# Optimization experiments

Measured on AMD Instinct MI355X. Metric: run time of the kernel, lower is better.

## Reference

```python
import jax, jax.numpy as jnp
import numpy as np

N_NODES = 50000
N_EDGES = 800000


def _sage_conv(h, ei, W_l, W_r, b_l):
    """PyG SAGEConv: lin_l(mean_{j->i} h_j) + lin_r(h_i). lin_l has bias, lin_r does not."""
    src, dst = ei[0], ei[1]
    # mean-aggregate raw features first (linear commutes with mean) to avoid [E, out] intermediates
    msum = jax.ops.segment_sum(h[src], dst, num_segments=N_NODES)          # [N, d]
    cnt = jax.ops.segment_sum(jnp.ones((ei.shape[1], 1), h.dtype), dst,
                              num_segments=N_NODES)                         # [N, 1]
    mean = msum / jnp.maximum(cnt, 1.0)
    return mean @ W_l + b_l + h @ W_r


def setup_inputs() -> dict:
    key = jax.random.key(0)
    ks = jax.random.split(key, 8)
    d_in, d_hid, d_out = 64, 64, 32
    return {
        "x": jax.random.normal(ks[0], (N_NODES, d_in), dtype=jnp.float32),
        "ei0": jax.random.randint(ks[1], (2, N_EDGES), 0, N_NODES, dtype=jnp.int32),
        "ei1": jax.random.randint(ks[2], (2, N_EDGES), 0, N_NODES, dtype=jnp.int32),
        "Wl": jax.random.normal(ks[3], (2, 2, d_in, d_hid), dtype=jnp.float32) * 0.05,
        "Wr": jax.random.normal(ks[4], (2, 2, d_in, d_hid), dtype=jnp.float32) * 0.05,
        "bl": jax.random.normal(ks[5], (2, 2, d_hid), dtype=jnp.float32) * 0.05,
        "lin_W": jax.random.normal(ks[6], (d_hid, d_out), dtype=jnp.float32) * 0.05,
        "lin_b": jax.random.normal(ks[7], (d_out,), dtype=jnp.float32) * 0.05,
    }


def reference(x, ei0, ei1, Wl, Wr, bl, lin_W, lin_b):
    edge_indices = (ei0, ei1)  # one edge_index per relation
    h = x
    for l in range(2):  # layers (structurally fixed)
        out = None
        for r, ei in enumerate(edge_indices):  # HeteroConv aggr='sum' over relations
            y = _sage_conv(h, ei, Wl[l, r], Wr[l, r], bl[l, r])
            out = y if out is None else out + y
        h = jax.nn.relu(out)
    return h @ lin_W + lin_b
```

## Files before the change

### kernel.cpp

```cpp
#include <hip/hip_runtime.h>

#define NN 50000
#define CAP 32
#define OVF_LDS 1024
#define SHARD_W 64
#define NSH 782
#define NPB 512

__device__ __forceinline__ unsigned short f2bf(float f) {
    unsigned u = __float_as_uint(f);
    u += 0x7fffu + ((u >> 16) & 1u);
    return (unsigned short)(u >> 16);
}
__device__ __forceinline__ float bf2f(unsigned short u) {
    return __uint_as_float(((unsigned)u) << 16);
}


__global__ __launch_bounds__(256) void shard_hist(
    const float* __restrict__ x, unsigned short* __restrict__ xb,
    const int* __restrict__ ei0, int E0,
    const int* __restrict__ ei1, int E1,
    unsigned short* __restrict__ hist16)
{
    int gtid = blockIdx.x * 256 + threadIdx.x;
    int gsz  = gridDim.x * 256;
    for (int i = gtid; i < NN * 16; i += gsz) {
        float4 v = ((const float4*)x)[i];
        ushort4 o;
        o.x = f2bf(v.x); o.y = f2bf(v.y); o.z = f2bf(v.z); o.w = f2bf(v.w);
        ((ushort4*)xb)[i] = o;
    }

    __shared__ unsigned lh[NSH];
    int local = blockIdx.x; int rel = 0;
    if (local >= NPB) { local -= NPB; rel = 1; }
    int pb = (local & 7) * (NPB / 8) + (local >> 3);
    const int* ei = rel ? ei1 : ei0;
    int E         = rel ? E1  : E0;
    int ce = (E + NPB - 1) / NPB;
    int lo = pb * ce, hi = min(lo + ce, E);

    for (int i = threadIdx.x; i < NSH; i += 256) lh[i] = 0;
    __syncthreads();
    for (int t = lo + threadIdx.x; t < hi; t += 256)
        atomicAdd(&lh[ei[E + t] >> 6], 1u);
    __syncthreads();
    for (int i = threadIdx.x; i < NSH; i += 256)
        hist16[((size_t)rel * NSH + i) * NPB + pb] = (unsigned short)lh[i];
}

__global__ __launch_bounds__(256) void total_pass(
    const unsigned short* __restrict__ hist16, int* __restrict__ tot)
{
    int gw = (blockIdx.x * 256 + threadIdx.x) >> 6;
    int lane = threadIdx.x & 63;
    if (gw >= 2 * NSH) return;
    uint4 v = ((const uint4*)(hist16 + (size_t)gw * NPB))[lane];
    unsigned s = (v.x & 0xffffu) + (v.x >> 16) + (v.y & 0xffffu) + (v.y >> 16)
               + (v.z & 0xffffu) + (v.z >> 16) + (v.w & 0xffffu) + (v.w >> 16);
    for (int off = 32; off; off >>= 1) s += __shfl_down(s, off);
    if (lane == 0) tot[gw] = (int)s;
}

__global__ __launch_bounds__(256) void scan_pass(
    const int* __restrict__ tot, int* __restrict__ sbase)
{
    __shared__ int ps[256];
    int t = threadIdx.x;
    int v[7];
    int s = 0;
    #pragma unroll
    for (int j = 0; j < 7; j++) {
        int i = t * 7 + j;
        v[j] = (i < 2 * NSH) ? tot[i] : 0;
        s += v[j];
    }
    ps[t] = s;
    __syncthreads();
    for (int off = 1; off < 256; off <<= 1) {
        int add = (t >= off) ? ps[t - off] : 0;
        __syncthreads();
        ps[t] += add;
        __syncthreads();
    }
    int run = (t == 0) ? 0 : ps[t - 1];
    #pragma unroll
    for (int j = 0; j < 7; j++) {
        int i = t * 7 + j;
        if (i < 2 * NSH) sbase[i] = run;
        run += v[j];
    }
    if (t == 255) sbase[2 * NSH] = run;
}

__global__ __launch_bounds__(256) void blockbase_pass(
    const unsigned short* __restrict__ hist16, const int* __restrict__ sbase,
    unsigned* __restrict__ pbase)
{
    int gw = (blockIdx.x * 256 + threadIdx.x) >> 6;
    int lane = threadIdx.x & 63;
    if (gw >= 2 * NSH) return;
    uint4 v = ((const uint4*)(hist16 + (size_t)gw * NPB))[lane];
    unsigned c[8] = {v.x & 0xffffu, v.x >> 16, v.y & 0xffffu, v.y >> 16,
                     v.z & 0xffffu, v.z >> 16, v.w & 0xffffu, v.w >> 16};
    unsigned lsum = 0;
    #pragma unroll
    for (int j = 0; j < 8; j++) lsum += c[j];
    unsigned incl = lsum;
    for (int off = 1; off < 64; off <<= 1) {
        unsigned n = __shfl_up(incl, off);
        if (lane >= off) incl += n;
    }
    unsigned run = (unsigned)sbase[gw] + incl - lsum;
    unsigned* prow = pbase + (size_t)gw * NPB + lane * 8;
    #pragma unroll
    for (int j = 0; j < 8; j++) { prow[j] = run; run += c[j]; }
}

__global__ __launch_bounds__(256) void partition_pass(
    const int* __restrict__ ei0, int E0,
    const int* __restrict__ ei1, int E1,
    const unsigned* __restrict__ pbase,
    unsigned* __restrict__ compact)
{
    __shared__ unsigned lbase[NSH];
    __shared__ unsigned lrank[NSH];
    int local = blockIdx.x; int rel = 0;
    if (local >= NPB) { local -= NPB; rel = 1; }
    int pb = (local & 7) * (NPB / 8) + (local >> 3);
    const int* ei = rel ? ei1 : ei0;
    int E         = rel ? E1  : E0;
    int ce = (E + NPB - 1) / NPB;
    int lo = pb * ce, hi = min(lo + ce, E);

    for (int i = threadIdx.x; i < NSH; i += 256) {
        lbase[i] = pbase[((size_t)rel * NSH + i) * NPB + pb];
        lrank[i] = 0;
    }
    __syncthreads();
    for (int t = lo + threadIdx.x; t < hi; t += 256) {
        int dst = ei[E + t];
        int src = ei[t];
        int s = dst >> 6;
        unsigned r = atomicAdd(&lrank[s], 1u);
        compact[lbase[s] + r] = ((unsigned)dst << 16) | (unsigned)src;
    }
}

__global__ __launch_bounds__(256) void aggregate_shard(
    const unsigned* __restrict__ compact, const int* __restrict__ sbase,
    const unsigned short* __restrict__ hb, unsigned short* __restrict__ agg)
{
    __shared__ unsigned short lbins[SHARD_W * CAP];
    __shared__ unsigned lcnt[SHARD_W];
    __shared__ unsigned lovf[OVF_LDS];
    __shared__ unsigned lovf_cnt;

    int bid = blockIdx.x;
    int rel = bid / NSH;
    int s   = bid - rel * NSH;
    int tid = threadIdx.x;
    int lane = tid & 63;
    int qtr = lane >> 4;
    int r   = lane & 15;
    int wid = tid >> 6;

    if (tid < SHARD_W) lcnt[tid] = 0;
    if (tid == 0) lovf_cnt = 0;
    __syncthreads();

    int base = sbase[bid];
    int tt   = sbase[bid + 1] - base;
    for (int j = tid; j < tt; j += 256) {
        unsigned e = compact[base + j];
        int loc = (int)(e >> 16) & (SHARD_W - 1);
        unsigned rr = atomicAdd(&lcnt[loc], 1u);
        if (rr < CAP) {
            lbins[loc * CAP + rr] = (unsigned short)(e & 0xffffu);
        } else {
            unsigned o = atomicAdd(&lovf_cnt, 1u);
            if (o < OVF_LDS) lovf[o] = ((unsigned)loc << 16) | (e & 0xffffu);
        }
    }
    __syncthreads();

    const uint2* hb64 = (const uint2*)hb;
    uint2* agg64 = (uint2*)agg;
    for (int t = 0; t < 16; ++t) {
        int loc = wid * 16 + t;
        int d = (int)lcnt[loc];
        int m = min(d, CAP);
        int idx = 0;
        if (lane < m) idx = lbins[loc * CAP + lane];
        float a0=0.f, a1=0.f, a2=0.f, a3=0.f;
        float b0=0.f, b1=0.f, b2=0.f, b3=0.f;
        int steps = (m + 3) >> 2;
        int j = 0;
        for (; j + 2 <= steps; j += 2) {
            int e0 = 4 * j + qtr;
            int e1 = 4 * (j + 1) + qtr;
            int s0 = __shfl(idx, e0 & 31);
            int s1 = __shfl(idx, e1 & 31);
            uint2 u0 = (e0 < m) ? hb64[(size_t)s0 * 16 + r] : make_uint2(0u, 0u);
            uint2 u1 = (e1 < m) ? hb64[(size_t)s1 * 16 + r] : make_uint2(0u, 0u);
            a0 += __uint_as_float(u0.x << 16); a1 += __uint_as_float(u0.x & 0xffff0000u);
            a2 += __uint_as_float(u0.y << 16); a3 += __uint_as_float(u0.y & 0xffff0000u);
            b0 += __uint_as_float(u1.x << 16); b1 += __uint_as_float(u1.x & 0xffff0000u);
            b2 += __uint_as_float(u1.y << 16); b3 += __uint_as_float(u1.y & 0xffff0000u);
        }
        for (; j < steps; ++j) {
            int e0 = 4 * j + qtr;
            int s0 = __shfl(idx, e0 & 31);
            uint2 u0 = (e0 < m) ? hb64[(size_t)s0 * 16 + r] : make_uint2(0u, 0u);
            a0 += __uint_as_float(u0.x << 16); a1 += __uint_as_float(u0.x & 0xffff0000u);
            a2 += __uint_as_float(u0.y << 16); a3 += __uint_as_float(u0.y & 0xffff0000u);
        }
        if (d > CAP) {
            int cnt = min((int)lovf_cnt, OVF_LDS);
            for (int e0 = 0; e0 < cnt; ++e0) {
                unsigned v = lovf[e0];
                if ((int)(v >> 16) == loc && qtr == 0) {
                    uint2 u = hb64[(size_t)(v & 0xffffu) * 16 + r];
                    a0 += __uint_as_float(u.x << 16); a1 += __uint_as_float(u.x & 0xffff0000u);
                    a2 += __uint_as_float(u.y << 16); a3 += __uint_as_float(u.y & 0xffff0000u);
                }
            }
        }
        a0 += b0; a1 += b1; a2 += b2; a3 += b3;
        a0 += __shfl_xor(a0, 16); a0 += __shfl_xor(a0, 32);
        a1 += __shfl_xor(a1, 16); a1 += __shfl_xor(a1, 32);
        a2 += __shfl_xor(a2, 16); a2 += __shfl_xor(a2, 32);
        a3 += __shfl_xor(a3, 16); a3 += __shfl_xor(a3, 32);
        int node = s * SHARD_W + loc;
        if (lane < 16 && node < NN) {
            float inv = 1.0f / (float)max(d, 1);
            uint2 o;
            o.x = (unsigned)f2bf(a0 * inv) | ((unsigned)f2bf(a1 * inv) << 16);
            o.y = (unsigned)f2bf(a2 * inv) | ((unsigned)f2bf(a3 * inv) << 16);
            agg64[((size_t)rel * NN + node) * 16 + r] = o;
        }
    }
}

#define RST 132
__global__ __launch_bounds__(256) void layer_gemm(
    const unsigned short* __restrict__ agg0, const unsigned short* __restrict__ agg1,
    const unsigned short* __restrict__ selfb,
    const float* __restrict__ Wl0, const float* __restrict__ Wl1,
    const float* __restrict__ Wr0, const float* __restrict__ Wr1,
    const float* __restrict__ b0, const float* __restrict__ b1,
    unsigned short* __restrict__ hb16)
{
    __shared__ float Wch[64 * 64];
    __shared__ float rowsT[64 * RST];
    __shared__ float bias[64];

    int tid = threadIdx.x;
    int base = blockIdx.x * 128;
    if (tid < 64) bias[tid] = b0[tid] + b1[tid];

    int j8 = (tid & 7) * 8;
    int n4 = (tid >> 3) * 4;

    float acc[4][8];
    #pragma unroll
    for (int i = 0; i < 4; i++)
        #pragma unroll
        for (int c = 0; c < 8; c++) acc[i][c] = 0.f;

    for (int chunk = 0; chunk < 3; chunk++) {
        const float* W = (chunk == 0) ? Wl0 : (chunk == 1) ? Wl1 : Wr0;
        const unsigned short* src = (chunk == 0) ? agg0 : (chunk == 1) ? agg1 : selfb;
        __syncthreads();
        #pragma unroll
        for (int r = 0; r < 4; r++) {
            int i = tid + 256 * r;
            float4 w = *(const float4*)&W[i * 4];
            if (chunk == 2) {
                float4 w2 = *(const float4*)&Wr1[i * 4];
                w.x += w2.x; w.y += w2.y; w.z += w2.z; w.w += w2.w;
            }
            *(float4*)&Wch[i * 4] = w;
        }
        #pragma unroll
        for (int r = 0; r < 8; r++) {
            int i = tid + 256 * r;
            int node = i >> 4;
            int k4 = (i & 15) * 4;
            int g = base + node;
            ushort4 u = make_ushort4(0, 0, 0, 0);
            if (g < NN) u = *(const ushort4*)&src[(size_t)g * 64 + k4];
            rowsT[(k4 + 0) * RST + node] = bf2f(u.x);
            rowsT[(k4 + 1) * RST + node] = bf2f(u.y);
            rowsT[(k4 + 2) * RST + node] = bf2f(u.z);
            rowsT[(k4 + 3) * RST + node] = bf2f(u.w);
        }
        __syncthreads();
        #pragma unroll 4
        for (int k = 0; k < 64; k++) {
            float4 wa = *(const float4*)&Wch[k * 64 + j8];
            float4 wb = *(const float4*)&Wch[k * 64 + j8 + 4];
            float4 rv = *(const float4*)&rowsT[k * RST + n4];
            float w[8] = {wa.x, wa.y, wa.z, wa.w, wb.x, wb.y, wb.z, wb.w};
            float rr[4] = {rv.x, rv.y, rv.z, rv.w};
            #pragma unroll
            for (int i = 0; i < 4; i++)
                #pragma unroll
                for (int c = 0; c < 8; c++)
                    acc[i][c] = fmaf(rr[i], w[c], acc[i][c]);
        }
    }

    #pragma unroll
    for (int i = 0; i < 4; i++) {
        int g = base + n4 + i;
        if (g < NN) {
            ushort4 p0, p1;
            p0.x = f2bf(fmaxf(acc[i][0] + bias[j8 + 0], 0.f));
            p0.y = f2bf(fmaxf(acc[i][1] + bias[j8 + 1], 0.f));
            p0.z = f2bf(fmaxf(acc[i][2] + bias[j8 + 2], 0.f));
            p0.w = f2bf(fmaxf(acc[i][3] + bias[j8 + 3], 0.f));
            p1.x = f2bf(fmaxf(acc[i][4] + bias[j8 + 4], 0.f));
            p1.y = f2bf(fmaxf(acc[i][5] + bias[j8 + 5], 0.f));
            p1.z = f2bf(fmaxf(acc[i][6] + bias[j8 + 6], 0.f));
            p1.w = f2bf(fmaxf(acc[i][7] + bias[j8 + 7], 0.f));
            *(ushort4*)&hb16[(size_t)g * 64 + j8]     = p0;
            *(ushort4*)&hb16[(size_t)g * 64 + j8 + 4] = p1;
        }
    }
}

__global__ __launch_bounds__(256) void layer_gemm_final(
    const unsigned short* __restrict__ agg0, const unsigned short* __restrict__ agg1,
    const unsigned short* __restrict__ selfb,
    const float* __restrict__ Wl0, const float* __restrict__ Wl1,
    const float* __restrict__ Wr0, const float* __restrict__ Wr1,
    const float* __restrict__ b0, const float* __restrict__ b1,
    const float* __restrict__ linW, const float* __restrict__ linb,
    float* __restrict__ out)
{
    __shared__ float Wch[64 * 64];
    __shared__ float rowsT[64 * RST];
    __shared__ float bias[64];

    int tid = threadIdx.x;
    int base = blockIdx.x * 128;
    if (tid < 64) bias[tid] = b0[tid] + b1[tid];

    int j8 = (tid & 7) * 8;
    int n4 = (tid >> 3) * 4;

    float acc[4][8];
    #pragma unroll
    for (int i = 0; i < 4; i++)
        #pragma unroll
        for (int c = 0; c < 8; c++) acc[i][c] = 0.f;

    for (int chunk = 0; chunk < 3; chunk++) {
        const float* W = (chunk == 0) ? Wl0 : (chunk == 1) ? Wl1 : Wr0;
        const unsigned short* src = (chunk == 0) ? agg0 : (chunk == 1) ? agg1 : selfb;
        __syncthreads();
        #pragma unroll
        for (int r = 0; r < 4; r++) {
            int i = tid + 256 * r;
            float4 w = *(const float4*)&W[i * 4];
            if (chunk == 2) {
                float4 w2 = *(const float4*)&Wr1[i * 4];
                w.x += w2.x; w.y += w2.y; w.z += w2.z; w.w += w2.w;
            }
            *(float4*)&Wch[i * 4] = w;
        }
        #pragma unroll
        for (int r = 0; r < 8; r++) {
            int i = tid + 256 * r;
            int node = i >> 4;
            int k4 = (i & 15) * 4;
            int g = base + node;
            ushort4 u = make_ushort4(0, 0, 0, 0);
            if (g < NN) u = *(const ushort4*)&src[(size_t)g * 64 + k4];
            rowsT[(k4 + 0) * RST + node] = bf2f(u.x);
            rowsT[(k4 + 1) * RST + node] = bf2f(u.y);
            rowsT[(k4 + 2) * RST + node] = bf2f(u.z);
            rowsT[(k4 + 3) * RST + node] = bf2f(u.w);
        }
        __syncthreads();
        #pragma unroll 4
        for (int k = 0; k < 64; k++) {
            float4 wa = *(const float4*)&Wch[k * 64 + j8];
            float4 wb = *(const float4*)&Wch[k * 64 + j8 + 4];
            float4 rv = *(const float4*)&rowsT[k * RST + n4];
            float w[8] = {wa.x, wa.y, wa.z, wa.w, wb.x, wb.y, wb.z, wb.w};
            float rr[4] = {rv.x, rv.y, rv.z, rv.w};
            #pragma unroll
            for (int i = 0; i < 4; i++)
                #pragma unroll
                for (int c = 0; c < 8; c++)
                    acc[i][c] = fmaf(rr[i], w[c], acc[i][c]);
        }
    }

    float o[4][8];
    #pragma unroll
    for (int i = 0; i < 4; i++)
        #pragma unroll
        for (int c = 0; c < 8; c++)
            o[i][c] = fmaxf(acc[i][c] + bias[j8 + c], 0.f);

    __syncthreads();

    #pragma unroll
    for (int r = 0; r < 2; r++) {
        int i = tid + 256 * r;
        *(float4*)&Wch[i * 4] = *(const float4*)&linW[i * 4];
    }
    if (tid < 32) bias[tid] = linb[tid];
    #pragma unroll
    for (int i = 0; i < 4; i++)
        #pragma unroll
        for (int c = 0; c < 8; c++)
            rowsT[(j8 + c) * RST + (n4 + i)] = o[i][c];
    __syncthreads();

    int j4 = (tid & 7) * 4;
    float acc2[4][4];
    #pragma unroll
    for (int i = 0; i < 4; i++)
        #pragma unroll
        for (int c = 0; c < 4; c++) acc2[i][c] = 0.f;
    #pragma unroll 4
    for (int k = 0; k < 64; k++) {
        float4 w = *(const float4*)&Wch[k * 32 + j4];
        float4 rv = *(const float4*)&rowsT[k * RST + n4];
        float wr[4] = {w.x, w.y, w.z, w.w};
        float rr[4] = {rv.x, rv.y, rv.z, rv.w};
        #pragma unroll
        for (int i = 0; i < 4; i++)
            #pragma unroll
            for (int c = 0; c < 4; c++)
                acc2[i][c] = fmaf(rr[i], wr[c], acc2[i][c]);
    }
    #pragma unroll
    for (int i = 0; i < 4; i++) {
        int g = base + n4 + i;
        if (g < NN) {
            float4 ov;
            ov.x = acc2[i][0] + bias[j4 + 0];
            ov.y = acc2[i][1] + bias[j4 + 1];
            ov.z = acc2[i][2] + bias[j4 + 2];
            ov.w = acc2[i][3] + bias[j4 + 3];
            *(float4*)&out[(size_t)g * 32 + j4] = ov;
        }
    }
}

extern "C" void kernel_launch(void* const* d_in, const int* in_sizes, int n_in,
                              void* d_out, int out_size, void* d_ws, size_t ws_size,
                              hipStream_t stream)
{
    const float* x    = (const float*)d_in[0];
    const int*   ei0  = (const int*)d_in[1];
    const int*   ei1  = (const int*)d_in[2];
    const float* Wl   = (const float*)d_in[3];
    const float* Wr   = (const float*)d_in[4];
    const float* bl   = (const float*)d_in[5];
    const float* linW = (const float*)d_in[6];
    const float* linb = (const float*)d_in[7];
    float* out = (float*)d_out;

    int E0 = in_sizes[1] / 2;
    int E1 = in_sizes[2] / 2;

    unsigned*       compact = (unsigned*)d_ws;
    unsigned short* h1b  = (unsigned short*)d_ws + (size_t)2 * NN * CAP;
    unsigned short* aggb = h1b + (size_t)NN * 64;
    unsigned short* agg0 = aggb;
    unsigned short* agg1 = aggb + (size_t)NN * 64;
    unsigned short* xb   = aggb + (size_t)2 * NN * 64;
    int*            tot   = (int*)(xb + (size_t)NN * 64);
    int*            sbase = tot + 2 * NSH;

    unsigned short* hist16 = aggb;
    unsigned*       pbase  = (unsigned*)(aggb + (size_t)2 * NSH * NPB);

    dim3 blk(256);
    int ggrid = (NN + 127) / 128;
    int wave_grid = (2 * NSH * 64 + 255) / 256;

    shard_hist<<<2 * NPB, blk, 0, stream>>>(x, xb, ei0, E0, ei1, E1, hist16);
    total_pass<<<wave_grid, blk, 0, stream>>>(hist16, tot);
    scan_pass<<<1, blk, 0, stream>>>(tot, sbase);
    blockbase_pass<<<wave_grid, blk, 0, stream>>>(hist16, sbase, pbase);
    partition_pass<<<2 * NPB, blk, 0, stream>>>(ei0, E0, ei1, E1, pbase, compact);

    aggregate_shard<<<2 * NSH, blk, 0, stream>>>(compact, sbase, xb, aggb);
    layer_gemm<<<ggrid, blk, 0, stream>>>(agg0, agg1, xb,
        Wl + 0, Wl + 4096, Wr + 0, Wr + 4096, bl + 0, bl + 64, h1b);

    aggregate_shard<<<2 * NSH, blk, 0, stream>>>(compact, sbase, h1b, aggb);
    layer_gemm_final<<<ggrid, blk, 0, stream>>>(agg0, agg1, h1b,
        Wl + 8192, Wl + 12288, Wr + 8192, Wr + 12288, bl + 128, bl + 192,
        linW, linb, out);
}
```

Baseline: 237.2 us.

## Fuse total and blockbase scan passes; widen aggregate gathers to 128-bit loads

The per-shard total pass and the block-base pass become one kernel that writes relative offsets plus shard totals. The global shard base is added later when partition_pass loads its offsets, which removes one launch and one read of the histogram. The aggregate kernel now has each lane load 16 bytes (8 bf16 features) per neighbor instead of 8, so 8 edges are gathered per wave step instead of 4. This costs more accumulator registers and an extra shuffle-reduction stage.

```diff
diff --git a/kernel.cpp b/kernel.cpp
--- a/kernel.cpp
+++ b/kernel.cpp
@@ -50,53 +50,10 @@
         hist16[((size_t)rel * NSH + i) * NPB + pb] = (unsigned short)lh[i];
 }
 
-__global__ __launch_bounds__(256) void total_pass(
-    const unsigned short* __restrict__ hist16, int* __restrict__ tot)
-{
-    int gw = (blockIdx.x * 256 + threadIdx.x) >> 6;
-    int lane = threadIdx.x & 63;
-    if (gw >= 2 * NSH) return;
-    uint4 v = ((const uint4*)(hist16 + (size_t)gw * NPB))[lane];
-    unsigned s = (v.x & 0xffffu) + (v.x >> 16) + (v.y & 0xffffu) + (v.y >> 16)
-               + (v.z & 0xffffu) + (v.z >> 16) + (v.w & 0xffffu) + (v.w >> 16);
-    for (int off = 32; off; off >>= 1) s += __shfl_down(s, off);
-    if (lane == 0) tot[gw] = (int)s;
-}
-
-__global__ __launch_bounds__(256) void scan_pass(
-    const int* __restrict__ tot, int* __restrict__ sbase)
-{
-    __shared__ int ps[256];
-    int t = threadIdx.x;
-    int v[7];
-    int s = 0;
-    #pragma unroll
-    for (int j = 0; j < 7; j++) {
-        int i = t * 7 + j;
-        v[j] = (i < 2 * NSH) ? tot[i] : 0;
-        s += v[j];
-    }
-    ps[t] = s;
-    __syncthreads();
-    for (int off = 1; off < 256; off <<= 1) {
-        int add = (t >= off) ? ps[t - off] : 0;
-        __syncthreads();
-        ps[t] += add;
-        __syncthreads();
-    }
-    int run = (t == 0) ? 0 : ps[t - 1];
-    #pragma unroll
-    for (int j = 0; j < 7; j++) {
-        int i = t * 7 + j;
-        if (i < 2 * NSH) sbase[i] = run;
-        run += v[j];
-    }
-    if (t == 255) sbase[2 * NSH] = run;
-}
-
-__global__ __launch_bounds__(256) void blockbase_pass(
-    const unsigned short* __restrict__ hist16, const int* __restrict__ sbase,
-    unsigned* __restrict__ pbase)
+__global__ __launch_bounds__(256) void blockbase_rel(
+    const unsigned short* __restrict__ hist16,
+    unsigned* __restrict__ pbase,
+    int* __restrict__ tot)
 {
     int gw = (blockIdx.x * 256 + threadIdx.x) >> 6;
     int lane = threadIdx.x & 63;
@@ -112,16 +69,48 @@
         unsigned n = __shfl_up(incl, off);
         if (lane >= off) incl += n;
     }
-    unsigned run = (unsigned)sbase[gw] + incl - lsum;
+    unsigned run = incl - lsum;
     unsigned* prow = pbase + (size_t)gw * NPB + lane * 8;
     #pragma unroll
     for (int j = 0; j < 8; j++) { prow[j] = run; run += c[j]; }
+    if (lane == 63) tot[gw] = (int)incl;
+}
+
+__global__ __launch_bounds__(256) void scan_pass(
+    const int* __restrict__ tot, int* __restrict__ sbase)
+{
+    __shared__ int ps[256];
+    int t = threadIdx.x;
+    int v[7];
+    int s = 0;
+    #pragma unroll
+    for (int j = 0; j < 7; j++) {
+        int i = t * 7 + j;
+        v[j] = (i < 2 * NSH) ? tot[i] : 0;
+        s += v[j];
+    }
+    ps[t] = s;
+    __syncthreads();
+    for (int off = 1; off < 256; off <<= 1) {
+        int add = (t >= off) ? ps[t - off] : 0;
+        __syncthreads();
+        ps[t] += add;
+        __syncthreads();
+    }
+    int run = (t == 0) ? 0 : ps[t - 1];
+    #pragma unroll
+    for (int j = 0; j < 7; j++) {
+        int i = t * 7 + j;
+        if (i < 2 * NSH) sbase[i] = run;
+        run += v[j];
+    }
+    if (t == 255) sbase[2 * NSH] = run;
 }
 
 __global__ __launch_bounds__(256) void partition_pass(
     const int* __restrict__ ei0, int E0,
     const int* __restrict__ ei1, int E1,
-    const unsigned* __restrict__ pbase,
+    const unsigned* __restrict__ pbase, const int* __restrict__ sbase,
     unsigned* __restrict__ compact)
 {
     __shared__ unsigned lbase[NSH];
@@ -135,7 +124,8 @@
     int lo = pb * ce, hi = min(lo + ce, E);
 
     for (int i = threadIdx.x; i < NSH; i += 256) {
-        lbase[i] = pbase[((size_t)rel * NSH + i) * NPB + pb];
+        lbase[i] = pbase[((size_t)rel * NSH + i) * NPB + pb]
+                 + (unsigned)sbase[rel * NSH + i];
         lrank[i] = 0;
     }
     __syncthreads();
@@ -162,8 +152,8 @@
     int s   = bid - rel * NSH;
     int tid = threadIdx.x;
     int lane = tid & 63;
-    int qtr = lane >> 4;
-    int r   = lane & 15;
+    int oct = lane >> 3;
+    int r   = lane & 7;
     int wid = tid >> 6;
 
     if (tid < SHARD_W) lcnt[tid] = 0;
@@ -185,60 +175,78 @@
     }
     __syncthreads();
 
-    const uint2* hb64 = (const uint2*)hb;
-    uint2* agg64 = (uint2*)agg;
+    const uint4* hb128 = (const uint4*)hb;
+    uint4* agg128 = (uint4*)agg;
     for (int t = 0; t < 16; ++t) {
         int loc = wid * 16 + t;
         int d = (int)lcnt[loc];
         int m = min(d, CAP);
         int idx = 0;
         if (lane < m) idx = lbins[loc * CAP + lane];
-        float a0=0.f, a1=0.f, a2=0.f, a3=0.f;
-        float b0=0.f, b1=0.f, b2=0.f, b3=0.f;
-        int steps = (m + 3) >> 2;
+        float a0=0.f,a1=0.f,a2=0.f,a3=0.f,a4=0.f,a5=0.f,a6=0.f,a7=0.f;
+        float b0=0.f,b1=0.f,b2=0.f,b3=0.f,b4=0.f,b5=0.f,b6=0.f,b7=0.f;
+        int steps = (m + 7) >> 3;
         int j = 0;
         for (; j + 2 <= steps; j += 2) {
-            int e0 = 4 * j + qtr;
-            int e1 = 4 * (j + 1) + qtr;
+            int e0 = 8 * j + oct;
+            int e1 = 8 * (j + 1) + oct;
             int s0 = __shfl(idx, e0 & 31);
             int s1 = __shfl(idx, e1 & 31);
-            uint2 u0 = (e0 < m) ? hb64[(size_t)s0 * 16 + r] : make_uint2(0u, 0u);
-            uint2 u1 = (e1 < m) ? hb64[(size_t)s1 * 16 + r] : make_uint2(0u, 0u);
+            uint4 u0 = (e0 < m) ? hb128[(size_t)s0 * 8 + r]
+                                : make_uint4(0u, 0u, 0u, 0u);
+            uint4 u1 = (e1 < m) ? hb128[(size_t)s1 * 8 + r]
+                                : make_uint4(0u, 0u, 0u, 0u);
             a0 += __uint_as_float(u0.x << 16); a1 += __uint_as_float(u0.x & 0xffff0000u);
             a2 += __uint_as_float(u0.y << 16); a3 += __uint_as_float(u0.y & 0xffff0000u);
+            a4 += __uint_as_float(u0.z << 16); a5 += __uint_as_float(u0.z & 0xffff0000u);
+            a6 += __uint_as_float(u0.w << 16); a7 += __uint_as_float(u0.w & 0xffff0000u);
             b0 += __uint_as_float(u1.x << 16); b1 += __uint_as_float(u1.x & 0xffff0000u);
             b2 += __uint_as_float(u1.y << 16); b3 += __uint_as_float(u1.y & 0xffff0000u);
+            b4 += __uint_as_float(u1.z << 16); b5 += __uint_as_float(u1.z & 0xffff0000u);
+            b6 += __uint_as_float(u1.w << 16); b7 += __uint_as_float(u1.w & 0xffff0000u);
         }
         for (; j < steps; ++j) {
-            int e0 = 4 * j + qtr;
+            int e0 = 8 * j + oct;
             int s0 = __shfl(idx, e0 & 31);
-            uint2 u0 = (e0 < m) ? hb64[(size_t)s0 * 16 + r] : make_uint2(0u, 0u);
+            uint4 u0 = (e0 < m) ? hb128[(size_t)s0 * 8 + r]
+                                : make_uint4(0u, 0u, 0u, 0u);
             a0 += __uint_as_float(u0.x << 16); a1 += __uint_as_float(u0.x & 0xffff0000u);
             a2 += __uint_as_float(u0.y << 16); a3 += __uint_as_float(u0.y & 0xffff0000u);
+            a4 += __uint_as_float(u0.z << 16); a5 += __uint_as_float(u0.z & 0xffff0000u);
+            a6 += __uint_as_float(u0.w << 16); a7 += __uint_as_float(u0.w & 0xffff0000u);
         }
         if (d > CAP) {
             int cnt = min((int)lovf_cnt, OVF_LDS);
             for (int e0 = 0; e0 < cnt; ++e0) {
                 unsigned v = lovf[e0];
-                if ((int)(v >> 16) == loc && qtr == 0) {
-                    uint2 u = hb64[(size_t)(v & 0xffffu) * 16 + r];
+                if ((int)(v >> 16) == loc && oct == 0) {
+                    uint4 u = hb128[(size_t)(v & 0xffffu) * 8 + r];
                     a0 += __uint_as_float(u.x << 16); a1 += __uint_as_float(u.x & 0xffff0000u);
                     a2 += __uint_as_float(u.y << 16); a3 += __uint_as_float(u.y & 0xffff0000u);
+                    a4 += __uint_as_float(u.z << 16); a5 += __uint_as_float(u.z & 0xffff0000u);
+                    a6 += __uint_as_float(u.w << 16); a7 += __uint_as_float(u.w & 0xffff0000u);
                 }
             }
         }
         a0 += b0; a1 += b1; a2 += b2; a3 += b3;
-        a0 += __shfl_xor(a0, 16); a0 += __shfl_xor(a0, 32);
-        a1 += __shfl_xor(a1, 16); a1 += __shfl_xor(a1, 32);
-        a2 += __shfl_xor(a2, 16); a2 += __shfl_xor(a2, 32);
-        a3 += __shfl_xor(a3, 16); a3 += __shfl_xor(a3, 32);
+        a4 += b4; a5 += b5; a6 += b6; a7 += b7;
+        a0 += __shfl_xor(a0, 8); a0 += __shfl_xor(a0, 16); a0 += __shfl_xor(a0, 32);
+        a1 += __shfl_xor(a1, 8); a1 += __shfl_xor(a1, 16); a1 += __shfl_xor(a1, 32);
+        a2 += __shfl_xor(a2, 8); a2 += __shfl_xor(a2, 16); a2 += __shfl_xor(a2, 32);
+        a3 += __shfl_xor(a3, 8); a3 += __shfl_xor(a3, 16); a3 += __shfl_xor(a3, 32);
+        a4 += __shfl_xor(a4, 8); a4 += __shfl_xor(a4, 16); a4 += __shfl_xor(a4, 32);
+        a5 += __shfl_xor(a5, 8); a5 += __shfl_xor(a5, 16); a5 += __shfl_xor(a5, 32);
+        a6 += __shfl_xor(a6, 8); a6 += __shfl_xor(a6, 16); a6 += __shfl_xor(a6, 32);
+        a7 += __shfl_xor(a7, 8); a7 += __shfl_xor(a7, 16); a7 += __shfl_xor(a7, 32);
         int node = s * SHARD_W + loc;
-        if (lane < 16 && node < NN) {
+        if (lane < 8 && node < NN) {
             float inv = 1.0f / (float)max(d, 1);
-            uint2 o;
+            uint4 o;
             o.x = (unsigned)f2bf(a0 * inv) | ((unsigned)f2bf(a1 * inv) << 16);
             o.y = (unsigned)f2bf(a2 * inv) | ((unsigned)f2bf(a3 * inv) << 16);
-            agg64[((size_t)rel * NN + node) * 16 + r] = o;
+            o.z = (unsigned)f2bf(a4 * inv) | ((unsigned)f2bf(a5 * inv) << 16);
+            o.w = (unsigned)f2bf(a6 * inv) | ((unsigned)f2bf(a7 * inv) << 16);
+            agg128[((size_t)rel * NN + node) * 8 + r] = o;
         }
     }
 }
@@ -488,10 +496,10 @@
     int wave_grid = (2 * NSH * 64 + 255) / 256;
 
     shard_hist<<<2 * NPB, blk, 0, stream>>>(x, xb, ei0, E0, ei1, E1, hist16);
-    total_pass<<<wave_grid, blk, 0, stream>>>(hist16, tot);
+    blockbase_rel<<<wave_grid, blk, 0, stream>>>(hist16, pbase, tot);
     scan_pass<<<1, blk, 0, stream>>>(tot, sbase);
-    blockbase_pass<<<wave_grid, blk, 0, stream>>>(hist16, sbase, pbase);
-    partition_pass<<<2 * NPB, blk, 0, stream>>>(ei0, E0, ei1, E1, pbase, compact);
+    partition_pass<<<2 * NPB, blk, 0, stream>>>(ei0, E0, ei1, E1, pbase, sbase,
+                                                compact);
 
     aggregate_shard<<<2 * NSH, blk, 0, stream>>>(compact, sbase, xb, aggb);
     layer_gemm<<<ggrid, blk, 0, stream>>>(agg0, agg1, xb,
```

New measurement: 246.6 us. +4.0%, slower.
